# Performance work log

Measured on AMD Instinct MI355X. Metric: run time of the kernel, lower is better.

## Reference

```python
import jax, jax.numpy as jnp
import numpy as np

D_MODEL = 2048
K_SIZE = 4
GROUPS = 2048  # depthwise


def setup_inputs() -> dict:
    key = jax.random.key(0)
    k1, k2, k3, k4 = jax.random.split(key, 4)
    B, S, D = 4, 4096, D_MODEL
    x = jax.random.normal(k1, (B, S, D), dtype=jnp.float32)
    # nn.Linear(d_model, 3*d_model, bias=False): weight [3D, D], y = x @ W.T
    w1 = jax.random.normal(k2, (3 * D, D), dtype=jnp.float32) * (1.0 / np.sqrt(D))
    w2 = jax.random.normal(k3, (D, D), dtype=jnp.float32) * (1.0 / np.sqrt(D))
    # nn.Conv1d depthwise weight: [out_ch=D, in_ch/groups=1, k]
    conv_w = jax.random.normal(k4, (D, 1, K_SIZE), dtype=jnp.float32) * (1.0 / np.sqrt(K_SIZE))
    return {"x": x, "w1": w1, "w2": w2, "conv_w": conv_w}


def reference(x, w1, w2, conv_w):
    # x: [B, S, D]
    BCx = jnp.einsum("bsd,ed->bse", x, w1)  # [B, S, 3D]
    Bg, Cg, Xg = jnp.split(BCx, 3, axis=-1)  # each [B, S, D]
    gated = Bg * Xg
    # depthwise causal conv: torch pads k-1 both sides then slices [:seq_len]
    # == left-pad only k-1 (causal)
    y = jax.lax.conv_general_dilated(
        gated.transpose(0, 2, 1),          # [B, D, S]
        conv_w,                            # [D, 1, K]
        window_strides=(1,),
        padding=[(K_SIZE - 1, 0)],
        feature_group_count=GROUPS,
        dimension_numbers=("NCH", "OIH", "NCH"),
    )                                       # [B, D, S]
    conv_out = y.transpose(0, 2, 1)         # [B, S, D]
    out = jnp.einsum("bsd,ed->bse", Cg * conv_out, w2)  # [B, S, D]
    return out
```

## Files before the change

kernel.cpp:

```cpp
#include <hip/hip_runtime.h>
#include <stdint.h>

typedef unsigned short u16;
typedef __bf16 bf16x8 __attribute__((ext_vector_type(8)));
typedef float  f32x4  __attribute__((ext_vector_type(4)));

#define D_MODEL 2048
#define SEQ     4096
#define NROWS   16384
#define THREE_D 6144
#define K_SIZE  4

__device__ __forceinline__ float b2f(u16 u) {
    union { uint32_t i; float f; } v; v.i = ((uint32_t)u) << 16; return v.f;
}
__device__ __forceinline__ u16 f2b(float f) {
    uint32_t u = __builtin_bit_cast(uint32_t, f);
    u += 0x7fff + ((u >> 16) & 1);
    return (u16)(u >> 16);
}

__global__ __launch_bounds__(256) void cast_f32_to_bf16(
    const float* __restrict__ src, u16* __restrict__ dst, int n8)
{
    int i = blockIdx.x * blockDim.x + threadIdx.x;
    if (i >= n8) return;
    const float4* s = (const float4*)src + (size_t)i * 2;
    float4 a = s[0], b = s[1];
    union { u16 u[8]; uint4 v; } o;
    o.u[0] = f2b(a.x); o.u[1] = f2b(a.y); o.u[2] = f2b(a.z); o.u[3] = f2b(a.w);
    o.u[4] = f2b(b.x); o.u[5] = f2b(b.y); o.u[6] = f2b(b.z); o.u[7] = f2b(b.w);
    *(uint4*)(dst + (size_t)i * 8) = o.v;
}

__global__ __launch_bounds__(256) void prep_cwt(
    const float* __restrict__ cw, float* __restrict__ cwt)
{
    int i = blockIdx.x * blockDim.x + threadIdx.x;
    if (i >= D_MODEL * K_SIZE) return;
    int d = i >> 2, k = i & 3;
    cwt[k * D_MODEL + d] = cw[i];
}

template<int BF16OUT>
__global__ __launch_bounds__(256, 3) void gemm_bt(
    const u16* __restrict__ A, const u16* __restrict__ B,
    void* __restrict__ Cout, int N, int K, int n_per_xcd)
{
    __shared__ u16 lA[128 * 64];
    __shared__ u16 lB[128 * 64];

    const int tid  = threadIdx.x;
    const int lane = tid & 63;
    const int wave = tid >> 6;
    const int wm = (wave >> 1) * 64;
    const int wn = (wave & 1) * 64;

    const int idx   = blockIdx.x;
    const int xcd   = idx & 7;
    const int local = idx >> 3;
    const int bm  = local / n_per_xcd;
    const int bn  = xcd * n_per_xcd + (local - bm * n_per_xcd);

    const int srow = lane >> 3;
    const int cg   = ((lane & 7) ^ srow) * 8;
    const size_t sK = (size_t)K;

    const u16* ga = A + ((size_t)(bm * 128) + wave * 8 + srow) * sK + cg;
    const u16* gb = B + ((size_t)(bn * 128) + wave * 8 + srow) * sK + cg;

    u16* lAw = lA + wave * 512;
    u16* lBw = lB + wave * 512;

    f32x4 acc[4][4] = {};

    const int fr = lane & 15;
    const int fq = lane >> 4;
    const int off0 = ((fq ^ (fr & 7)) * 8);
    const int off1 = off0 ^ 32;

    for (int kk = 0; kk < K; kk += 64) {
        #pragma unroll
        for (int p = 0; p < 4; p++) {
            __builtin_amdgcn_global_load_lds(
                (const __attribute__((address_space(1))) void*)(ga + (size_t)p * 32 * sK + kk),
                (__attribute__((address_space(3))) void*)(lAw + p * 2048), 16, 0, 0);
            __builtin_amdgcn_global_load_lds(
                (const __attribute__((address_space(1))) void*)(gb + (size_t)p * 32 * sK + kk),
                (__attribute__((address_space(3))) void*)(lBw + p * 2048), 16, 0, 0);
        }
        __syncthreads();

        bf16x8 a0[4], b0[4], a1[4], b1[4];
        #pragma unroll
        for (int i = 0; i < 4; i++) {
            a0[i] = *(const bf16x8*)&lA[(wm + i * 16 + fr) * 64 + off0];
            b0[i] = *(const bf16x8*)&lB[(wn + i * 16 + fr) * 64 + off0];
        }
        #pragma unroll
        for (int i = 0; i < 4; i++) {
            a1[i] = *(const bf16x8*)&lA[(wm + i * 16 + fr) * 64 + off1];
            b1[i] = *(const bf16x8*)&lB[(wn + i * 16 + fr) * 64 + off1];
        }

        #pragma unroll
        for (int i = 0; i < 4; i++)
            #pragma unroll
            for (int j = 0; j < 4; j++)
                acc[i][j] = __builtin_amdgcn_mfma_f32_16x16x32_bf16(
                    a0[i], b0[j], acc[i][j], 0, 0, 0);
        #pragma unroll
        for (int i = 0; i < 4; i++)
            #pragma unroll
            for (int j = 0; j < 4; j++)
                acc[i][j] = __builtin_amdgcn_mfma_f32_16x16x32_bf16(
                    a1[i], b1[j], acc[i][j], 0, 0, 0);

        __syncthreads();
    }

    const int row0 = bm * 128 + wm + fq * 4;
    const int col0 = bn * 128 + wn + fr;
    if (BF16OUT) {
        u16* C = (u16*)Cout;
        #pragma unroll
        for (int i = 0; i < 4; i++)
            #pragma unroll
            for (int j = 0; j < 4; j++)
                #pragma unroll
                for (int r = 0; r < 4; r++)
                    C[(size_t)(row0 + i * 16 + r) * N + (col0 + j * 16)] = f2b(acc[i][j][r]);
    } else {
        float* C = (float*)Cout;
        #pragma unroll
        for (int i = 0; i < 4; i++)
            #pragma unroll
            for (int j = 0; j < 4; j++)
                #pragma unroll
                for (int r = 0; r < 4; r++)
                    C[(size_t)(row0 + i * 16 + r) * N + (col0 + j * 16)] = acc[i][j][r];
    }
}

__global__ __launch_bounds__(256) void gate_conv(
    const u16* __restrict__ BCx, const float* __restrict__ cwt, u16* __restrict__ z)
{
    const int n  = blockIdx.x;
    const int dg = threadIdx.x << 3;
    const int s  = n & (SEQ - 1);
    const u16* base = BCx + (size_t)n * THREE_D;

    float conv[8];
    #pragma unroll
    for (int j = 0; j < 8; j++) conv[j] = 0.f;

    #pragma unroll
    for (int r = 0; r < 4; r++) {
        const int back = 3 - r;
        if (s >= back) {
            const u16* pb = base - (size_t)back * THREE_D + dg;
            union { uint4 v; u16 u[8]; } ub, ux;
            ub.v = *(const uint4*)pb;
            ux.v = *(const uint4*)(pb + 2 * D_MODEL);
            const float* w = cwt + r * D_MODEL + dg;
            float4 w0 = *(const float4*)w;
            float4 w1 = *(const float4*)(w + 4);
            float ww[8] = { w0.x, w0.y, w0.z, w0.w, w1.x, w1.y, w1.z, w1.w };
            #pragma unroll
            for (int j = 0; j < 8; j++)
                conv[j] += b2f(ub.u[j]) * b2f(ux.u[j]) * ww[j];
        }
    }

    union { uint4 v; u16 u[8]; } uc, uo;
    uc.v = *(const uint4*)(base + D_MODEL + dg);
    #pragma unroll
    for (int j = 0; j < 8; j++)
        uo.u[j] = f2b(b2f(uc.u[j]) * conv[j]);
    *(uint4*)(z + (size_t)n * D_MODEL + dg) = uo.v;
}

extern "C" void kernel_launch(void* const* d_in, const int* in_sizes, int n_in,
                              void* d_out, int out_size, void* d_ws, size_t ws_size,
                              hipStream_t stream) {
    const float* x  = (const float*)d_in[0];
    const float* w1 = (const float*)d_in[1];
    const float* w2 = (const float*)d_in[2];
    const float* cw = (const float*)d_in[3];
    float* out = (float*)d_out;

    char* ws = (char*)d_ws;
    u16*   xb  = (u16*)(ws);
    u16*   w1b = (u16*)(ws + 67108864);
    u16*   w2b = (u16*)(ws + 92274688);
    float* cwt = (float*)(ws + 100663296);
    u16*   bcx = (u16*)(ws + 100696064);
    u16*   z   = (u16*)(ws + 302022656);

    cast_f32_to_bf16<<<dim3((4194304 + 255) / 256), 256, 0, stream>>>(x,  xb,  4194304);
    cast_f32_to_bf16<<<dim3((1572864 + 255) / 256), 256, 0, stream>>>(w1, w1b, 1572864);
    cast_f32_to_bf16<<<dim3((524288  + 255) / 256), 256, 0, stream>>>(w2, w2b, 524288);
    prep_cwt<<<dim3(32), 256, 0, stream>>>(cw, cwt);

    gemm_bt<1><<<dim3(128 * 48), 256, 0, stream>>>(xb, w1b, (void*)bcx, THREE_D, D_MODEL, 6);
    gate_conv<<<dim3(NROWS), 256, 0, stream>>>(bcx, cwt, z);
    gemm_bt<0><<<dim3(128 * 16), 256, 0, stream>>>(z, w2b, (void*)out, D_MODEL, D_MODEL, 2);
}
```

Measured before the change: 874.0 us.

## Replace GEMM with 256x256-tile, 512-thread, 4-stage pipelined LDS kernel

Result: slower. 933.3 us (+6.8%).

```diff
diff --git a/kernel.cpp b/kernel.cpp
--- a/kernel.cpp
+++ b/kernel.cpp
@@ -10,6 +10,8 @@
 #define NROWS   16384
 #define THREE_D 6144
 #define K_SIZE  4
+#define KC      2048
+#define NT      64
 
 __device__ __forceinline__ float b2f(u16 u) {
     union { uint32_t i; float f; } v; v.i = ((uint32_t)u) << 16; return v.f;
@@ -42,19 +44,20 @@
     cwt[k * D_MODEL + d] = cw[i];
 }
 
+#define GLDS(gp, lp) __builtin_amdgcn_global_load_lds( \
+    (const __attribute__((address_space(1))) void*)(gp), \
+    (__attribute__((address_space(3))) void*)(lp), 16, 0, 0)
+
 template<int BF16OUT>
-__global__ __launch_bounds__(256, 3) void gemm_bt(
+__global__ __launch_bounds__(512, 2) void gemm256(
     const u16* __restrict__ A, const u16* __restrict__ B,
-    void* __restrict__ Cout, int N, int K, int n_per_xcd)
-{
-    __shared__ u16 lA[128 * 64];
-    __shared__ u16 lB[128 * 64];
+    void* __restrict__ Cout, int N, int n_per_xcd)
+{
+    __shared__ __align__(16) u16 lds[65536];
 
     const int tid  = threadIdx.x;
     const int lane = tid & 63;
     const int wave = tid >> 6;
-    const int wm = (wave >> 1) * 64;
-    const int wn = (wave & 1) * 64;
 
     const int idx   = blockIdx.x;
     const int xcd   = idx & 7;
@@ -62,69 +65,86 @@
     const int bm  = local / n_per_xcd;
     const int bn  = xcd * n_per_xcd + (local - bm * n_per_xcd);
 
-    const int srow = lane >> 3;
-    const int cg   = ((lane & 7) ^ srow) * 8;
-    const size_t sK = (size_t)K;
-
-    const u16* ga = A + ((size_t)(bm * 128) + wave * 8 + srow) * sK + cg;
-    const u16* gb = B + ((size_t)(bn * 128) + wave * 8 + srow) * sK + cg;
-
-    u16* lAw = lA + wave * 512;
-    u16* lBw = lB + wave * 512;
-
-    f32x4 acc[4][4] = {};
+    const int sfr  = tid & 15;
+    const int sfq  = (tid >> 4) & 3;
+    const int srow = (tid >> 6) * 16 + sfr;
+    const size_t sK = (size_t)KC;
+    const u16* ga = A + ((size_t)(bm * 256) + srow) * sK + sfq * 8;
+    const u16* gb = B + ((size_t)(bn * 256) + srow) * sK + sfq * 8;
+
+    u16* dst0 = lds + wave * 512;
 
     const int fr = lane & 15;
     const int fq = lane >> 4;
-    const int off0 = ((fq ^ (fr & 7)) * 8);
-    const int off1 = off0 ^ 32;
-
-    for (int kk = 0; kk < K; kk += 64) {
-        #pragma unroll
-        for (int p = 0; p < 4; p++) {
-            __builtin_amdgcn_global_load_lds(
-                (const __attribute__((address_space(1))) void*)(ga + (size_t)p * 32 * sK + kk),
-                (__attribute__((address_space(3))) void*)(lAw + p * 2048), 16, 0, 0);
-            __builtin_amdgcn_global_load_lds(
-                (const __attribute__((address_space(1))) void*)(gb + (size_t)p * 32 * sK + kk),
-                (__attribute__((address_space(3))) void*)(lBw + p * 2048), 16, 0, 0);
+    const int wm = (wave >> 2) * 128;
+    const int wn = (wave & 3) * 64;
+    const int aBase = (wave >> 2) * 4096 + fq * 128 + fr * 8;
+    const int bBase = 8192 + (wave & 3) * 2048 + fq * 128 + fr * 8;
+
+    f32x4 acc[8][4] = {};
+
+    #pragma unroll
+    for (int t = 0; t < 3; t++) {
+        u16* d = dst0 + t * 16384;
+        const int kk = t * 32;
+        GLDS(ga + kk,            d);
+        GLDS(ga + 128 * sK + kk, d + 4096);
+        GLDS(gb + kk,            d + 8192);
+        GLDS(gb + 128 * sK + kk, d + 12288);
+        __builtin_amdgcn_sched_barrier(0);
+    }
+    asm volatile("s_waitcnt vmcnt(8)" ::: "memory");
+    __builtin_amdgcn_s_barrier();
+    __builtin_amdgcn_sched_barrier(0);
+
+    for (int t = 0; t < NT; t++) {
+        const int buf = t & 3;
+        if (t + 3 < NT) {
+            u16* d = dst0 + ((t + 3) & 3) * 16384;
+            const int kk = (t + 3) * 32;
+            GLDS(ga + kk,            d);
+            GLDS(ga + 128 * sK + kk, d + 4096);
+            GLDS(gb + kk,            d + 8192);
+            GLDS(gb + 128 * sK + kk, d + 12288);
         }
-        __syncthreads();
-
-        bf16x8 a0[4], b0[4], a1[4], b1[4];
-        #pragma unroll
-        for (int i = 0; i < 4; i++) {
-            a0[i] = *(const bf16x8*)&lA[(wm + i * 16 + fr) * 64 + off0];
-            b0[i] = *(const bf16x8*)&lB[(wn + i * 16 + fr) * 64 + off0];
-        }
-        #pragma unroll
-        for (int i = 0; i < 4; i++) {
-            a1[i] = *(const bf16x8*)&lA[(wm + i * 16 + fr) * 64 + off1];
-            b1[i] = *(const bf16x8*)&lB[(wn + i * 16 + fr) * 64 + off1];
-        }
-
-        #pragma unroll
-        for (int i = 0; i < 4; i++)
+        __builtin_amdgcn_sched_barrier(0);
+
+        bf16x8 a[8], b[4];
+        const u16* la = lds + buf * 16384 + aBase;
+        const u16* lb = lds + buf * 16384 + bBase;
+        #pragma unroll
+        for (int i = 0; i < 8; i++) a[i] = *(const bf16x8*)(la + i * 512);
+        #pragma unroll
+        for (int j = 0; j < 4; j++) b[j] = *(const bf16x8*)(lb + j * 512);
+
+        __builtin_amdgcn_s_setprio(1);
+        #pragma unroll
+        for (int i = 0; i < 8; i++)
             #pragma unroll
             for (int j = 0; j < 4; j++)
                 acc[i][j] = __builtin_amdgcn_mfma_f32_16x16x32_bf16(
-                    a0[i], b0[j], acc[i][j], 0, 0, 0);
-        #pragma unroll
-        for (int i = 0; i < 4; i++)
-            #pragma unroll
-            for (int j = 0; j < 4; j++)
-                acc[i][j] = __builtin_amdgcn_mfma_f32_16x16x32_bf16(
-                    a1[i], b1[j], acc[i][j], 0, 0, 0);
-
-        __syncthreads();
-    }
-
-    const int row0 = bm * 128 + wm + fq * 4;
-    const int col0 = bn * 128 + wn + fr;
+                    a[i], b[j], acc[i][j], 0, 0, 0);
+        __builtin_amdgcn_s_setprio(0);
+
+        asm volatile("s_waitcnt lgkmcnt(0)" ::: "memory");
+        __builtin_amdgcn_sched_barrier(0);
+        if (t < NT - 3) {
+            asm volatile("s_waitcnt vmcnt(8)" ::: "memory");
+        } else if (t == NT - 3) {
+            asm volatile("s_waitcnt vmcnt(4)" ::: "memory");
+        } else if (t == NT - 2) {
+            asm volatile("s_waitcnt vmcnt(0)" ::: "memory");
+        }
+        __builtin_amdgcn_s_barrier();
+        __builtin_amdgcn_sched_barrier(0);
+    }
+
+    const int row0 = bm * 256 + wm + fq * 4;
+    const int col0 = bn * 256 + wn + fr;
     if (BF16OUT) {
         u16* C = (u16*)Cout;
         #pragma unroll
-        for (int i = 0; i < 4; i++)
+        for (int i = 0; i < 8; i++)
             #pragma unroll
             for (int j = 0; j < 4; j++)
                 #pragma unroll
@@ -133,7 +153,7 @@
     } else {
         float* C = (float*)Cout;
         #pragma unroll
-        for (int i = 0; i < 4; i++)
+        for (int i = 0; i < 8; i++)
             #pragma unroll
             for (int j = 0; j < 4; j++)
                 #pragma unroll
@@ -202,7 +222,7 @@
     cast_f32_to_bf16<<<dim3((524288  + 255) / 256), 256, 0, stream>>>(w2, w2b, 524288);
     prep_cwt<<<dim3(32), 256, 0, stream>>>(cw, cwt);
 
-    gemm_bt<1><<<dim3(128 * 48), 256, 0, stream>>>(xb, w1b, (void*)bcx, THREE_D, D_MODEL, 6);
+    gemm256<1><<<dim3(1536), 512, 0, stream>>>(xb, w1b, (void*)bcx, THREE_D, 3);
     gate_conv<<<dim3(NROWS), 256, 0, stream>>>(bcx, cwt, z);
-    gemm_bt<0><<<dim3(128 * 16), 256, 0, stream>>>(z, w2b, (void*)out, D_MODEL, D_MODEL, 2);
-}
+    gemm256<0><<<dim3(512), 512, 0, stream>>>(z, w2b, (void*)out, D_MODEL, 1);
+}
```
